# Optimization experiments

Hardware: AMD Instinct MI355X
Metric: run time of the kernel (lower is better)

Reference implementation:

```python
import jax, jax.numpy as jnp
import numpy as np

N = 10000      # atoms
E = 320000     # edges (avg degree 32)
H = 128        # hidden_channels
NH = 8         # num_heads
HD = H // NH   # head_dim
CUTOFF = 5.0


def setup_inputs() -> dict:
    key = jax.random.key(0)
    ks = jax.random.split(key, 32)
    s = 0.05
    x = jax.random.normal(ks[0], (N, H), dtype=jnp.float32)
    vec = jax.random.normal(ks[1], (N, 3, H), dtype=jnp.float32) * 0.1
    edge_index = jax.random.randint(ks[2], (2, E), 0, N, dtype=jnp.int64)
    r_ij = jax.random.uniform(ks[3], (E,), dtype=jnp.float32) * CUTOFF
    f_ij = jax.random.normal(ks[4], (E, H), dtype=jnp.float32)
    d = jax.random.normal(ks[5], (E, 3), dtype=jnp.float32)
    d_ij = d / jnp.linalg.norm(d, axis=-1, keepdims=True)
    def w(k, shape):
        return jax.random.normal(k, shape, dtype=jnp.float32) * s
    params = dict(
        Wq=w(ks[6], (H, H)), bq=jnp.zeros((H,), jnp.float32),
        Wk=w(ks[7], (H, H)), bk=jnp.zeros((H,), jnp.float32),
        Wv=w(ks[8], (H, H)), bv=jnp.zeros((H,), jnp.float32),
        Wdk=w(ks[9], (H, H)), bdk=jnp.zeros((H,), jnp.float32),
        Wdv=w(ks[10], (H, H)), bdv=jnp.zeros((H,), jnp.float32),
        Wvec=w(ks[11], (H, 3 * H)),
        Ws=w(ks[12], (H, 2 * H)), bs=jnp.zeros((2 * H,), jnp.float32),
        Wo=w(ks[13], (H, 3 * H)), bo=jnp.zeros((3 * H,), jnp.float32),
        Wf=w(ks[14], (H, 2 * H)), bf=jnp.zeros((2 * H,), jnp.float32),
        Wwsrc=w(ks[15], (H, H)), Wwtrg=w(ks[16], (H, H)),
        Wtsrc=w(ks[17], (H, H)), Wttrg=w(ks[18], (H, H)),
    )
    return dict(x=x, vec=vec, edge_index=edge_index, r_ij=r_ij,
                f_ij=f_ij, d_ij=d_ij, **params)


def _cosine_cutoff(r):
    return 0.5 * (jnp.cos(r * (jnp.pi / CUTOFF)) + 1.0) * (r < CUTOFF)


def _vector_rejection(v, d):
    # v: [E,3,H], d: [E,3]
    vp = jnp.sum(v * d[:, :, None], axis=1, keepdims=True)  # [E,1,H]
    return v - vp * d[:, :, None]


def reference(x, vec, edge_index, r_ij, f_ij, d_ij,
              Wq, bq, Wk, bk, Wv, bv, Wdk, bdk, Wdv, bdv, Wvec,
              Ws, bs, Wo, bo, Wf, bf, Wwsrc, Wwtrg, Wtsrc, Wttrg):
    silu = jax.nn.silu
    src, dst = edge_index[0], edge_index[1]  # j = source, i = target

    q = (x @ Wq + bq).reshape(-1, NH, HD)
    k = (x @ Wk + bk).reshape(-1, NH, HD)
    v = (x @ Wv + bv).reshape(-1, NH, HD)
    dk = silu(f_ij @ Wdk + bdk).reshape(-1, NH, HD)
    dv = silu(f_ij @ Wdv + bdv).reshape(-1, NH, HD)

    vec1, vec2, vec3 = jnp.split(vec @ Wvec, 3, axis=-1)  # each [N,3,H]
    vec_dot = jnp.sum(vec1 * vec2, axis=1)  # [N,H]

    # message
    attn = jnp.sum(q[dst] * k[src] * dk, axis=-1)          # [E,NH]
    attn = silu(attn) * _cosine_cutoff(r_ij)[:, None]       # [E,NH]
    vj = (v[src] * dv * attn[:, :, None]).reshape(-1, H)    # [E,H]
    s1, s2 = jnp.split(silu(vj @ Ws + bs), 2, axis=-1)
    vec_msg = vec[src] * s1[:, None, :] + s2[:, None, :] * d_ij[:, :, None]  # [E,3,H]

    # aggregate (scatter-add at target node)
    x_agg = jax.ops.segment_sum(vj, dst, num_segments=N)          # [N,H]
    vec_agg = jax.ops.segment_sum(vec_msg, dst, num_segments=N)   # [N,3,H]

    o1, o2, o3 = jnp.split(x_agg @ Wo + bo, 3, axis=-1)
    dx = vec_dot * o2 + o3
    dvec = vec3 * o1[:, None, :] + vec_agg

    # edge update
    vi, vj_full = vec[dst], vec[src]
    w1 = _vector_rejection(vi @ Wwtrg, d_ij)
    w2 = _vector_rejection(vj_full @ Wwsrc, -d_ij)
    w_dot = jnp.sum(w1 * w2, axis=1)  # [E,H]
    t1 = _vector_rejection(vi @ Wttrg, d_ij)
    t2 = _vector_rejection(vi @ Wtsrc, -d_ij)
    t_dot = jnp.sum(t1 * t2, axis=1)  # [E,H]
    f1, f2 = jnp.split(silu(f_ij @ Wf + bf), 2, axis=-1)
    df_ij = f1 * w_dot + f2 * t_dot

    return dx, dvec, df_ij
```

## Files before the change

### kernel.cpp

```cpp
#include <hip/hip_runtime.h>
#include <math.h>

#define NATOM 10000
#define NEDGE 320000
#define HDIM  128
#define NHEAD 8

__device__ __forceinline__ float silu_f(float x) {
    return x / (1.0f + expf(-x));
}

__global__ __launch_bounds__(256) void k_zero4(float4* __restrict__ p, int n4) {
    int i = blockIdx.x * 256 + threadIdx.x;
    if (i < n4) p[i] = float4{0.f, 0.f, 0.f, 0.f};
}

__global__ __launch_bounds__(256) void k_node_qkv(
    const float* __restrict__ x,
    const float* __restrict__ Wq, const float* __restrict__ bq,
    const float* __restrict__ Wk, const float* __restrict__ bk,
    const float* __restrict__ Wv, const float* __restrict__ bv,
    float* __restrict__ q, float* __restrict__ k, float* __restrict__ v)
{
    __shared__ float xs[8 * HDIM];
    int base = blockIdx.x * 8;
    reinterpret_cast<float4*>(xs)[threadIdx.x] =
        reinterpret_cast<const float4*>(x + (size_t)base * HDIM)[threadIdx.x];
    __syncthreads();
    int h = threadIdx.x & 127, half = threadIdx.x >> 7;
    float aq[4], ak[4], av[4];
#pragma unroll
    for (int i = 0; i < 4; ++i) { aq[i] = bq[h]; ak[i] = bk[h]; av[i] = bv[h]; }
    for (int kk = 0; kk < HDIM; ++kk) {
        float wq = Wq[kk * HDIM + h], wk = Wk[kk * HDIM + h], wv = Wv[kk * HDIM + h];
#pragma unroll
        for (int i = 0; i < 4; ++i) {
            float xv = xs[(half + 2 * i) * HDIM + kk];
            aq[i] = fmaf(xv, wq, aq[i]);
            ak[i] = fmaf(xv, wk, ak[i]);
            av[i] = fmaf(xv, wv, av[i]);
        }
    }
#pragma unroll
    for (int i = 0; i < 4; ++i) {
        int node = base + half + 2 * i;
        q[(size_t)node * HDIM + h] = aq[i];
        k[(size_t)node * HDIM + h] = ak[i];
        v[(size_t)node * HDIM + h] = av[i];
    }
}

__global__ __launch_bounds__(256) void k_node_vec(
    const float* __restrict__ vec,
    const float* __restrict__ Wvec,
    const float* __restrict__ Wwtrg, const float* __restrict__ Wwsrc,
    const float* __restrict__ Wttrg, const float* __restrict__ Wtsrc,
    float* __restrict__ vecdot, float* __restrict__ vec3o,
    float* __restrict__ vwt, float* __restrict__ vws,
    float* __restrict__ vtt, float* __restrict__ vts)
{
    __shared__ float vs[8 * 3 * HDIM];
    int base = blockIdx.x * 8;
    {
        const float4* vg = reinterpret_cast<const float4*>(vec + (size_t)base * 3 * HDIM);
        float4* vs4 = reinterpret_cast<float4*>(vs);
        for (int t = threadIdx.x; t < 768; t += 256) vs4[t] = vg[t];
    }
    __syncthreads();
    int h = threadIdx.x & 127, half = threadIdx.x >> 7;
    float vdot[4] = {0.f, 0.f, 0.f, 0.f};
    for (int s = 0; s < 3; ++s) {
        float a1[4] = {0,0,0,0}, a2[4] = {0,0,0,0}, a3[4] = {0,0,0,0};
        float awt[4] = {0,0,0,0}, aws[4] = {0,0,0,0}, att[4] = {0,0,0,0}, ats[4] = {0,0,0,0};
        for (int kk = 0; kk < HDIM; ++kk) {
            float w1 = Wvec[kk * 384 + h];
            float w2 = Wvec[kk * 384 + HDIM + h];
            float w3 = Wvec[kk * 384 + 2 * HDIM + h];
            float wwt = Wwtrg[kk * HDIM + h];
            float wws = Wwsrc[kk * HDIM + h];
            float wtt = Wttrg[kk * HDIM + h];
            float wts = Wtsrc[kk * HDIM + h];
#pragma unroll
            for (int i = 0; i < 4; ++i) {
                float vv = vs[((half + 2 * i) * 3 + s) * HDIM + kk];
                a1[i]  = fmaf(vv, w1, a1[i]);
                a2[i]  = fmaf(vv, w2, a2[i]);
                a3[i]  = fmaf(vv, w3, a3[i]);
                awt[i] = fmaf(vv, wwt, awt[i]);
                aws[i] = fmaf(vv, wws, aws[i]);
                att[i] = fmaf(vv, wtt, att[i]);
                ats[i] = fmaf(vv, wts, ats[i]);
            }
        }
#pragma unroll
        for (int i = 0; i < 4; ++i) {
            int node = base + half + 2 * i;
            size_t ob = ((size_t)node * 3 + s) * HDIM + h;
            vdot[i] += a1[i] * a2[i];
            vec3o[ob] = a3[i];
            vwt[ob] = awt[i];
            vws[ob] = aws[i];
            vtt[ob] = att[i];
            vts[ob] = ats[i];
        }
    }
#pragma unroll
    for (int i = 0; i < 4; ++i)
        vecdot[(size_t)(base + half + 2 * i) * HDIM + h] = vdot[i];
}

__global__ __launch_bounds__(256) void k_edge_fused(
    const float* __restrict__ fij, const int* __restrict__ eidx,
    const float* __restrict__ rij, const float* __restrict__ dij,
    const float* __restrict__ q, const float* __restrict__ k, const float* __restrict__ v,
    const float* __restrict__ vec,
    const float* __restrict__ Wdk, const float* __restrict__ bdk,
    const float* __restrict__ Wdv, const float* __restrict__ bdv,
    const float* __restrict__ Ws, const float* __restrict__ bs,
    float* __restrict__ xagg, float* __restrict__ dvec)
{
    __shared__ float ldsA[16 * 256];
    __shared__ float ldsW[32 * 256];
    __shared__ int   srcS[64], dstS[64];
    __shared__ float rcutS[64];
    __shared__ float dS[64][3];

    int e0 = blockIdx.x * 64;
    if (threadIdx.x < 64) {
        srcS[threadIdx.x] = eidx[e0 + threadIdx.x];
        dstS[threadIdx.x] = eidx[NEDGE + e0 + threadIdx.x];
        float r = rij[e0 + threadIdx.x];
        rcutS[threadIdx.x] = (r < 5.0f) ? 0.5f * (cosf(r * 0.6283185307179586f) + 1.0f) : 0.0f;
    }
    if (threadIdx.x < 192) ((float*)dS)[threadIdx.x] = dij[(size_t)e0 * 3 + threadIdx.x];

    int tx = threadIdx.x & 31, ty = threadIdx.x >> 5;
    float acc[8][8];
#pragma unroll
    for (int i = 0; i < 8; ++i)
#pragma unroll
        for (int j = 0; j < 8; ++j) acc[i][j] = 0.f;

    for (int kc = 0; kc < 4; ++kc) {
#pragma unroll
        for (int it = 0; it < 2; ++it) {
            int f4 = threadIdx.x + it * 256;
            int m = f4 >> 3, c4 = f4 & 7;
            reinterpret_cast<float4*>(ldsA)[f4] =
                *reinterpret_cast<const float4*>(&fij[(size_t)(e0 + m) * HDIM + kc * 32 + c4 * 4]);
        }
#pragma unroll
        for (int it = 0; it < 8; ++it) {
            int f4 = threadIdx.x + it * 256;
            int kk = f4 >> 6, oc4 = f4 & 63;
            int o = oc4 * 4;
            const float* sp = (o < HDIM) ? &Wdk[(size_t)(kc * 32 + kk) * HDIM + o]
                                         : &Wdv[(size_t)(kc * 32 + kk) * HDIM + (o - HDIM)];
            reinterpret_cast<float4*>(ldsW)[f4] = *reinterpret_cast<const float4*>(sp);
        }
        __syncthreads();
#pragma unroll 4
        for (int kk = 0; kk < 32; ++kk) {
            float a[8], b[8];
#pragma unroll
            for (int i = 0; i < 8; ++i) a[i] = ldsA[(ty * 8 + i) * 32 + kk];
#pragma unroll
            for (int j = 0; j < 8; ++j) b[j] = ldsW[kk * 256 + tx + 32 * j];
#pragma unroll
            for (int i = 0; i < 8; ++i)
#pragma unroll
                for (int j = 0; j < 8; ++j) acc[i][j] = fmaf(a[i], b[j], acc[i][j]);
        }
        __syncthreads();
    }

    float bdk_r[4], bdv_r[4];
#pragma unroll
    for (int j = 0; j < 4; ++j) {
        int c = tx + 32 * j;
        bdk_r[j] = bdk[c];
        bdv_r[j] = bdv[c];
    }

    float attn[8][4];
#pragma unroll
    for (int i = 0; i < 8; ++i) {
        int m = ty * 8 + i;
        int sn = srcS[m], dn = dstS[m];
        float rc = rcutS[m];
#pragma unroll
        for (int j = 0; j < 4; ++j) {
            int c = tx + 32 * j;
            float dk = silu_f(acc[i][j] + bdk_r[j]);
            float p = q[(size_t)dn * HDIM + c] * k[(size_t)sn * HDIM + c] * dk;
            p += __shfl_xor(p, 1);
            p += __shfl_xor(p, 2);
            p += __shfl_xor(p, 4);
            p += __shfl_xor(p, 8);
            attn[i][j] = silu_f(p) * rc;
        }
    }

#pragma unroll
    for (int i = 0; i < 8; ++i) {
        int m = ty * 8 + i;
        int sn = srcS[m], dn = dstS[m];
#pragma unroll
        for (int j = 0; j < 4; ++j) {
            int c = tx + 32 * j;
            float dv = silu_f(acc[i][j + 4] + bdv_r[j]);
            float val = v[(size_t)sn * HDIM + c] * dv * attn[i][j];
            ldsW[m * HDIM + c] = val;
            atomicAdd(&xagg[(size_t)dn * HDIM + c], val);
        }
    }
    __syncthreads();

#pragma unroll
    for (int i = 0; i < 8; ++i)
#pragma unroll
        for (int j = 0; j < 8; ++j) acc[i][j] = 0.f;

    for (int kc = 0; kc < 8; ++kc) {
#pragma unroll
        for (int it = 0; it < 4; ++it) {
            int f4 = threadIdx.x + it * 256;
            int kk = f4 >> 6, oc4 = f4 & 63;
            reinterpret_cast<float4*>(ldsA)[f4] =
                reinterpret_cast<const float4*>(Ws)[(size_t)(kc * 16 + kk) * 64 + oc4];
        }
        __syncthreads();
#pragma unroll 4
        for (int kk = 0; kk < 16; ++kk) {
            float a[8], b[8];
#pragma unroll
            for (int i = 0; i < 8; ++i) a[i] = ldsW[(ty * 8 + i) * HDIM + kc * 16 + kk];
#pragma unroll
            for (int j = 0; j < 8; ++j) b[j] = ldsA[kk * 256 + tx + 32 * j];
#pragma unroll
            for (int i = 0; i < 8; ++i)
#pragma unroll
                for (int j = 0; j < 8; ++j) acc[i][j] = fmaf(a[i], b[j], acc[i][j]);
        }
        __syncthreads();
    }

    float bs1[4], bs2[4];
#pragma unroll
    for (int j = 0; j < 4; ++j) {
        int c = tx + 32 * j;
        bs1[j] = bs[c];
        bs2[j] = bs[HDIM + c];
    }
#pragma unroll
    for (int i = 0; i < 8; ++i) {
        int m = ty * 8 + i;
        int dn = dstS[m], sn = srcS[m];
        float d0 = dS[m][0], d1 = dS[m][1], d2 = dS[m][2];
#pragma unroll
        for (int j = 0; j < 4; ++j) {
            int c = tx + 32 * j;
            float s1 = silu_f(acc[i][j] + bs1[j]);
            float s2 = silu_f(acc[i][j + 4] + bs2[j]);
            size_t vb = (size_t)sn * 3 * HDIM + c;
            size_t ab = (size_t)dn * 3 * HDIM + c;
            atomicAdd(&dvec[ab],            fmaf(vec[vb],            s1, s2 * d0));
            atomicAdd(&dvec[ab + HDIM],     fmaf(vec[vb + HDIM],     s1, s2 * d1));
            atomicAdd(&dvec[ab + 2 * HDIM], fmaf(vec[vb + 2 * HDIM], s1, s2 * d2));
        }
    }
}

__global__ __launch_bounds__(256) void k_node_out(
    const float* __restrict__ xagg,
    const float* __restrict__ vecdot, const float* __restrict__ vec3o,
    const float* __restrict__ Wo, const float* __restrict__ bo,
    float* __restrict__ dx, float* __restrict__ dvec)
{
    __shared__ float xs[8 * HDIM];
    int base = blockIdx.x * 8;
    reinterpret_cast<float4*>(xs)[threadIdx.x] =
        reinterpret_cast<const float4*>(xagg + (size_t)base * HDIM)[threadIdx.x];
    __syncthreads();
    int h = threadIdx.x & 127, half = threadIdx.x >> 7;
    float o1[4], o2[4], o3[4];
#pragma unroll
    for (int i = 0; i < 4; ++i) { o1[i] = bo[h]; o2[i] = bo[HDIM + h]; o3[i] = bo[2 * HDIM + h]; }
    for (int kk = 0; kk < HDIM; ++kk) {
        float w1 = Wo[kk * 384 + h], w2 = Wo[kk * 384 + HDIM + h], w3 = Wo[kk * 384 + 2 * HDIM + h];
#pragma unroll
        for (int i = 0; i < 4; ++i) {
            float xv = xs[(half + 2 * i) * HDIM + kk];
            o1[i] = fmaf(xv, w1, o1[i]);
            o2[i] = fmaf(xv, w2, o2[i]);
            o3[i] = fmaf(xv, w3, o3[i]);
        }
    }
#pragma unroll
    for (int i = 0; i < 4; ++i) {
        int node = base + half + 2 * i;
        dx[(size_t)node * HDIM + h] = fmaf(vecdot[(size_t)node * HDIM + h], o2[i], o3[i]);
        size_t vb = (size_t)node * 3 * HDIM + h;
#pragma unroll
        for (int s = 0; s < 3; ++s)
            dvec[vb + s * HDIM] = fmaf(vec3o[vb + s * HDIM], o1[i], dvec[vb + s * HDIM]);
    }
}

__global__ __launch_bounds__(256) void k_edge_df(
    const float* __restrict__ fij, const int* __restrict__ eidx,
    const float* __restrict__ dij,
    const float* __restrict__ Wf, const float* __restrict__ bf,
    const float* __restrict__ vwt, const float* __restrict__ vws,
    const float* __restrict__ vtt, const float* __restrict__ vts,
    float* __restrict__ dfo)
{
    __shared__ float ldsA[64 * HDIM];
    __shared__ float ldsW[16 * 256];
    __shared__ int   srcS[64], dstS[64];
    __shared__ float dS[64][3];

    int e0 = blockIdx.x * 64;
    if (threadIdx.x < 64) {
        srcS[threadIdx.x] = eidx[e0 + threadIdx.x];
        dstS[threadIdx.x] = eidx[NEDGE + e0 + threadIdx.x];
    }
    if (threadIdx.x < 192) ((float*)dS)[threadIdx.x] = dij[(size_t)e0 * 3 + threadIdx.x];
#pragma unroll
    for (int it = 0; it < 8; ++it) {
        int f4 = threadIdx.x + it * 256;
        reinterpret_cast<float4*>(ldsA)[f4] =
            reinterpret_cast<const float4*>(fij + (size_t)e0 * HDIM)[f4];
    }
    __syncthreads();

    int tx = threadIdx.x & 31, ty = threadIdx.x >> 5;
    float acc[8][8];
#pragma unroll
    for (int i = 0; i < 8; ++i)
#pragma unroll
        for (int j = 0; j < 8; ++j) acc[i][j] = 0.f;

    for (int kc = 0; kc < 8; ++kc) {
#pragma unroll
        for (int it = 0; it < 4; ++it) {
            int f4 = threadIdx.x + it * 256;
            int kk = f4 >> 6, oc4 = f4 & 63;
            reinterpret_cast<float4*>(ldsW)[f4] =
                reinterpret_cast<const float4*>(Wf)[(size_t)(kc * 16 + kk) * 64 + oc4];
        }
        __syncthreads();
#pragma unroll 4
        for (int kk = 0; kk < 16; ++kk) {
            float a[8], b[8];
#pragma unroll
            for (int i = 0; i < 8; ++i) a[i] = ldsA[(ty * 8 + i) * HDIM + kc * 16 + kk];
#pragma unroll
            for (int j = 0; j < 8; ++j) b[j] = ldsW[kk * 256 + tx + 32 * j];
#pragma unroll
            for (int i = 0; i < 8; ++i)
#pragma unroll
                for (int j = 0; j < 8; ++j) acc[i][j] = fmaf(a[i], b[j], acc[i][j]);
        }
        __syncthreads();
    }
    float bf1[4], bf2[4];
#pragma unroll
    for (int j = 0; j < 4; ++j) {
        int c = tx + 32 * j;
        bf1[j] = bf[c];
        bf2[j] = bf[HDIM + c];
    }
#pragma unroll
    for (int i = 0; i < 8; ++i) {
        int m = ty * 8 + i;
        int dn = dstS[m], sn = srcS[m];
        float d0 = dS[m][0], d1 = dS[m][1], d2 = dS[m][2];
#pragma unroll
        for (int j = 0; j < 4; ++j) {
            int c = tx + 32 * j;
            float f1 = silu_f(acc[i][j] + bf1[j]);
            float f2 = silu_f(acc[i][j + 4] + bf2[j]);
            size_t db = (size_t)dn * 3 * HDIM + c;
            size_t sb = (size_t)sn * 3 * HDIM + c;
            float a0 = vwt[db], a1 = vwt[db + HDIM], a2 = vwt[db + 2 * HDIM];
            float b0 = vws[sb], b1 = vws[sb + HDIM], b2 = vws[sb + 2 * HDIM];
            float t10 = vtt[db], t11 = vtt[db + HDIM], t12 = vtt[db + 2 * HDIM];
            float t20 = vts[db], t21 = vts[db + HDIM], t22 = vts[db + 2 * HDIM];
            float A  = a0 * d0 + a1 * d1 + a2 * d2;
            float B  = b0 * d0 + b1 * d1 + b2 * d2;
            float P1 = t10 * d0 + t11 * d1 + t12 * d2;
            float P2 = t20 * d0 + t21 * d1 + t22 * d2;
            float wdot = a0 * b0 + a1 * b1 + a2 * b2 - A * B;
            float tdot = t10 * t20 + t11 * t21 + t12 * t22 - P1 * P2;
            dfo[(size_t)(e0 + m) * HDIM + c] = f1 * wdot + f2 * tdot;
        }
    }
}

extern "C" void kernel_launch(void* const* d_in, const int* in_sizes, int n_in,
                              void* d_out, int out_size, void* d_ws, size_t ws_size,
                              hipStream_t stream)
{
    const float* x     = (const float*)d_in[0];
    const float* vec   = (const float*)d_in[1];
    const int*   eidx  = (const int*)d_in[2];
    const float* rij   = (const float*)d_in[3];
    const float* fij   = (const float*)d_in[4];
    const float* dij   = (const float*)d_in[5];
    const float* Wq    = (const float*)d_in[6];
    const float* bq    = (const float*)d_in[7];
    const float* Wk    = (const float*)d_in[8];
    const float* bk    = (const float*)d_in[9];
    const float* Wv    = (const float*)d_in[10];
    const float* bv    = (const float*)d_in[11];
    const float* Wdk   = (const float*)d_in[12];
    const float* bdk   = (const float*)d_in[13];
    const float* Wdv   = (const float*)d_in[14];
    const float* bdv   = (const float*)d_in[15];
    const float* Wvec  = (const float*)d_in[16];
    const float* Ws    = (const float*)d_in[17];
    const float* bs    = (const float*)d_in[18];
    const float* Wo    = (const float*)d_in[19];
    const float* bo    = (const float*)d_in[20];
    const float* Wf    = (const float*)d_in[21];
    const float* bf    = (const float*)d_in[22];
    const float* Wwsrc = (const float*)d_in[23];
    const float* Wwtrg = (const float*)d_in[24];
    const float* Wtsrc = (const float*)d_in[25];
    const float* Wttrg = (const float*)d_in[26];

    float* ws = (float*)d_ws;
    size_t o = 0;
    float* q      = ws + o; o += (size_t)NATOM * HDIM;
    float* kf     = ws + o; o += (size_t)NATOM * HDIM;
    float* vf     = ws + o; o += (size_t)NATOM * HDIM;
    float* vecdot = ws + o; o += (size_t)NATOM * HDIM;
    float* vec3o  = ws + o; o += (size_t)NATOM * 3 * HDIM;
    float* vwt    = ws + o; o += (size_t)NATOM * 3 * HDIM;
    float* vws_   = ws + o; o += (size_t)NATOM * 3 * HDIM;
    float* vtt    = ws + o; o += (size_t)NATOM * 3 * HDIM;
    float* vts    = ws + o; o += (size_t)NATOM * 3 * HDIM;
    float* xagg   = ws + o; o += (size_t)NATOM * HDIM;

    float* dx   = (float*)d_out;
    float* dvec = dx + (size_t)NATOM * HDIM;
    float* dfo  = dvec + (size_t)NATOM * 3 * HDIM;

    hipLaunchKernelGGL(k_zero4, dim3((NATOM * HDIM / 4 + 255) / 256), dim3(256), 0, stream,
                       (float4*)xagg, NATOM * HDIM / 4);
    hipLaunchKernelGGL(k_zero4, dim3((NATOM * 3 * HDIM / 4 + 255) / 256), dim3(256), 0, stream,
                       (float4*)dvec, NATOM * 3 * HDIM / 4);
    hipLaunchKernelGGL(k_node_qkv, dim3(NATOM / 8), dim3(256), 0, stream,
                       x, Wq, bq, Wk, bk, Wv, bv, q, kf, vf);
    hipLaunchKernelGGL(k_node_vec, dim3(NATOM / 8), dim3(256), 0, stream,
                       vec, Wvec, Wwtrg, Wwsrc, Wttrg, Wtsrc,
                       vecdot, vec3o, vwt, vws_, vtt, vts);
    hipLaunchKernelGGL(k_edge_fused, dim3(NEDGE / 64), dim3(256), 0, stream,
                       fij, eidx, rij, dij, q, kf, vf, vec,
                       Wdk, bdk, Wdv, bdv, Ws, bs, xagg, dvec);
    hipLaunchKernelGGL(k_node_out, dim3(NATOM / 8), dim3(256), 0, stream,
                       xagg, vecdot, vec3o, Wo, bo, dx, dvec);
    hipLaunchKernelGGL(k_edge_df, dim3(NEDGE / 64), dim3(256), 0, stream,
                       fij, eidx, dij, Wf, bf, vwt, vws_, vtt, vts, dfo);
}
```

Before: 1.689 ms.

## Fuse edge kernels and run edge GEMMs on bf16x3 split MFMA

Merges the two edge kernels into one, so f_ij is read and converted only once per edge tile. The three per-edge GEMMs (Wf, Wdk/Wdv and Ws) move from scalar FP32 FMA loops to MFMA 16x16x32 bf16 instructions. Inputs and weights are split into high and low bf16 parts, and three products are summed to keep near-FP32 accuracy. A prep kernel converts and transposes the weights each call. This trades more MFMA work and LDS conversion for far cheaper matrix math and one fewer kernel launch.

```diff
diff --git a/kernel.cpp b/kernel.cpp
--- a/kernel.cpp
+++ b/kernel.cpp
@@ -6,13 +6,47 @@
 #define HDIM  128
 #define NHEAD 8
 
+typedef short  v8s  __attribute__((ext_vector_type(8)));
+typedef float  v4f  __attribute__((ext_vector_type(4)));
+
 __device__ __forceinline__ float silu_f(float x) {
     return x / (1.0f + expf(-x));
+}
+
+__device__ __forceinline__ short f2bf(float x) {
+    union { float f; unsigned u; } c; c.f = x;
+    unsigned r = (c.u + 0x7FFF + ((c.u >> 16) & 1)) >> 16;
+    return (short)r;
+}
+__device__ __forceinline__ float bf2f(short h) {
+    union { unsigned u; float f; } c; c.u = ((unsigned)(unsigned short)h) << 16;
+    return c.f;
 }
 
 __global__ __launch_bounds__(256) void k_zero4(float4* __restrict__ p, int n4) {
     int i = blockIdx.x * 256 + threadIdx.x;
     if (i < n4) p[i] = float4{0.f, 0.f, 0.f, 0.f};
+}
+
+__global__ __launch_bounds__(128) void k_prep(
+    const float* __restrict__ Wdk, const float* __restrict__ Wdv,
+    const float* __restrict__ Ws,  const float* __restrict__ Wf,
+    short* __restrict__ WmsgH, short* __restrict__ WmsgL,
+    short* __restrict__ WstH,  short* __restrict__ WstL,
+    short* __restrict__ WftH,  short* __restrict__ WftL)
+{
+    int b = blockIdx.x;
+    int mat = b >> 8, n = b & 255, k = threadIdx.x;
+    float x;
+    if (mat == 0) x = (n < HDIM) ? Wdk[k * HDIM + n] : Wdv[k * HDIM + (n - HDIM)];
+    else if (mat == 1) x = Ws[k * 256 + n];
+    else x = Wf[k * 256 + n];
+    short h = f2bf(x);
+    short l = f2bf(x - bf2f(h));
+    short* H = (mat == 0) ? WmsgH : (mat == 1) ? WstH : WftH;
+    short* L = (mat == 0) ? WmsgL : (mat == 1) ? WstL : WftL;
+    H[n * HDIM + k] = h;
+    L[n * HDIM + k] = l;
 }
 
 __global__ __launch_bounds__(256) void k_node_qkv(
@@ -109,164 +143,194 @@
         vecdot[(size_t)(base + half + 2 * i) * HDIM + h] = vdot[i];
 }
 
-__global__ __launch_bounds__(256) void k_edge_fused(
+__device__ __forceinline__ void gemm_split(
+    const short* asHp, const short* asLp,
+    const short* __restrict__ WH, const short* __restrict__ WL,
+    const int* colbase, int n16, int q8, v4f acc[4][4])
+{
+#pragma unroll
+    for (int kc = 0; kc < 4; ++kc) {
+        v8s aH[4], aL[4];
+#pragma unroll
+        for (int mt = 0; mt < 4; ++mt) {
+            int off = (mt * 16 + n16) * 136 + kc * 32 + q8 * 8;
+            aH[mt] = *reinterpret_cast<const v8s*>(asHp + off);
+            aL[mt] = *reinterpret_cast<const v8s*>(asLp + off);
+        }
+#pragma unroll
+        for (int nt = 0; nt < 4; ++nt) {
+            size_t woff = (size_t)(colbase[nt] + n16) * HDIM + kc * 32 + q8 * 8;
+            v8s bH = *reinterpret_cast<const v8s*>(WH + woff);
+            v8s bL = *reinterpret_cast<const v8s*>(WL + woff);
+#pragma unroll
+            for (int mt = 0; mt < 4; ++mt) {
+                acc[mt][nt] = __builtin_amdgcn_mfma_f32_16x16x32_bf16(aH[mt], bL, acc[mt][nt], 0, 0, 0);
+                acc[mt][nt] = __builtin_amdgcn_mfma_f32_16x16x32_bf16(aL[mt], bH, acc[mt][nt], 0, 0, 0);
+                acc[mt][nt] = __builtin_amdgcn_mfma_f32_16x16x32_bf16(aH[mt], bH, acc[mt][nt], 0, 0, 0);
+            }
+        }
+    }
+}
+
+__global__ __launch_bounds__(256) void k_edge_mega(
     const float* __restrict__ fij, const int* __restrict__ eidx,
     const float* __restrict__ rij, const float* __restrict__ dij,
     const float* __restrict__ q, const float* __restrict__ k, const float* __restrict__ v,
     const float* __restrict__ vec,
-    const float* __restrict__ Wdk, const float* __restrict__ bdk,
-    const float* __restrict__ Wdv, const float* __restrict__ bdv,
-    const float* __restrict__ Ws, const float* __restrict__ bs,
-    float* __restrict__ xagg, float* __restrict__ dvec)
-{
-    __shared__ float ldsA[16 * 256];
-    __shared__ float ldsW[32 * 256];
+    const short* __restrict__ WmsgH, const short* __restrict__ WmsgL,
+    const short* __restrict__ WstH,  const short* __restrict__ WstL,
+    const short* __restrict__ WftH,  const short* __restrict__ WftL,
+    const float* __restrict__ bdk, const float* __restrict__ bdv,
+    const float* __restrict__ bs,  const float* __restrict__ bfb,
+    const float* __restrict__ vwt, const float* __restrict__ vws,
+    const float* __restrict__ vtt, const float* __restrict__ vts,
+    float* __restrict__ xagg, float* __restrict__ dvec, float* __restrict__ dfo)
+{
+    __shared__ short asH[64 * 136];
+    __shared__ short asL[64 * 136];
     __shared__ int   srcS[64], dstS[64];
-    __shared__ float rcutS[64];
-    __shared__ float dS[64][3];
+    __shared__ float rcutS[64], d0S[64], d1S[64], d2S[64];
 
     int e0 = blockIdx.x * 64;
     if (threadIdx.x < 64) {
-        srcS[threadIdx.x] = eidx[e0 + threadIdx.x];
-        dstS[threadIdx.x] = eidx[NEDGE + e0 + threadIdx.x];
-        float r = rij[e0 + threadIdx.x];
-        rcutS[threadIdx.x] = (r < 5.0f) ? 0.5f * (cosf(r * 0.6283185307179586f) + 1.0f) : 0.0f;
-    }
-    if (threadIdx.x < 192) ((float*)dS)[threadIdx.x] = dij[(size_t)e0 * 3 + threadIdx.x];
-
-    int tx = threadIdx.x & 31, ty = threadIdx.x >> 5;
-    float acc[8][8];
-#pragma unroll
-    for (int i = 0; i < 8; ++i)
-#pragma unroll
-        for (int j = 0; j < 8; ++j) acc[i][j] = 0.f;
-
-    for (int kc = 0; kc < 4; ++kc) {
-#pragma unroll
-        for (int it = 0; it < 2; ++it) {
-            int f4 = threadIdx.x + it * 256;
-            int m = f4 >> 3, c4 = f4 & 7;
-            reinterpret_cast<float4*>(ldsA)[f4] =
-                *reinterpret_cast<const float4*>(&fij[(size_t)(e0 + m) * HDIM + kc * 32 + c4 * 4]);
-        }
-#pragma unroll
-        for (int it = 0; it < 8; ++it) {
-            int f4 = threadIdx.x + it * 256;
-            int kk = f4 >> 6, oc4 = f4 & 63;
-            int o = oc4 * 4;
-            const float* sp = (o < HDIM) ? &Wdk[(size_t)(kc * 32 + kk) * HDIM + o]
-                                         : &Wdv[(size_t)(kc * 32 + kk) * HDIM + (o - HDIM)];
-            reinterpret_cast<float4*>(ldsW)[f4] = *reinterpret_cast<const float4*>(sp);
-        }
-        __syncthreads();
-#pragma unroll 4
-        for (int kk = 0; kk < 32; ++kk) {
-            float a[8], b[8];
-#pragma unroll
-            for (int i = 0; i < 8; ++i) a[i] = ldsA[(ty * 8 + i) * 32 + kk];
-#pragma unroll
-            for (int j = 0; j < 8; ++j) b[j] = ldsW[kk * 256 + tx + 32 * j];
-#pragma unroll
-            for (int i = 0; i < 8; ++i)
-#pragma unroll
-                for (int j = 0; j < 8; ++j) acc[i][j] = fmaf(a[i], b[j], acc[i][j]);
-        }
-        __syncthreads();
-    }
-
-    float bdk_r[4], bdv_r[4];
-#pragma unroll
-    for (int j = 0; j < 4; ++j) {
-        int c = tx + 32 * j;
-        bdk_r[j] = bdk[c];
-        bdv_r[j] = bdv[c];
-    }
-
-    float attn[8][4];
-#pragma unroll
-    for (int i = 0; i < 8; ++i) {
-        int m = ty * 8 + i;
-        int sn = srcS[m], dn = dstS[m];
-        float rc = rcutS[m];
-#pragma unroll
-        for (int j = 0; j < 4; ++j) {
-            int c = tx + 32 * j;
-            float dk = silu_f(acc[i][j] + bdk_r[j]);
-            float p = q[(size_t)dn * HDIM + c] * k[(size_t)sn * HDIM + c] * dk;
-            p += __shfl_xor(p, 1);
-            p += __shfl_xor(p, 2);
-            p += __shfl_xor(p, 4);
-            p += __shfl_xor(p, 8);
-            attn[i][j] = silu_f(p) * rc;
-        }
-    }
-
-#pragma unroll
-    for (int i = 0; i < 8; ++i) {
-        int m = ty * 8 + i;
-        int sn = srcS[m], dn = dstS[m];
-#pragma unroll
-        for (int j = 0; j < 4; ++j) {
-            int c = tx + 32 * j;
-            float dv = silu_f(acc[i][j + 4] + bdv_r[j]);
-            float val = v[(size_t)sn * HDIM + c] * dv * attn[i][j];
-            ldsW[m * HDIM + c] = val;
-            atomicAdd(&xagg[(size_t)dn * HDIM + c], val);
-        }
-    }
-    __syncthreads();
-
-#pragma unroll
-    for (int i = 0; i < 8; ++i)
-#pragma unroll
-        for (int j = 0; j < 8; ++j) acc[i][j] = 0.f;
-
-    for (int kc = 0; kc < 8; ++kc) {
-#pragma unroll
-        for (int it = 0; it < 4; ++it) {
-            int f4 = threadIdx.x + it * 256;
-            int kk = f4 >> 6, oc4 = f4 & 63;
-            reinterpret_cast<float4*>(ldsA)[f4] =
-                reinterpret_cast<const float4*>(Ws)[(size_t)(kc * 16 + kk) * 64 + oc4];
-        }
-        __syncthreads();
-#pragma unroll 4
-        for (int kk = 0; kk < 16; ++kk) {
-            float a[8], b[8];
-#pragma unroll
-            for (int i = 0; i < 8; ++i) a[i] = ldsW[(ty * 8 + i) * HDIM + kc * 16 + kk];
-#pragma unroll
-            for (int j = 0; j < 8; ++j) b[j] = ldsA[kk * 256 + tx + 32 * j];
-#pragma unroll
-            for (int i = 0; i < 8; ++i)
-#pragma unroll
-                for (int j = 0; j < 8; ++j) acc[i][j] = fmaf(a[i], b[j], acc[i][j]);
-        }
-        __syncthreads();
-    }
-
-    float bs1[4], bs2[4];
-#pragma unroll
-    for (int j = 0; j < 4; ++j) {
-        int c = tx + 32 * j;
-        bs1[j] = bs[c];
-        bs2[j] = bs[HDIM + c];
-    }
-#pragma unroll
-    for (int i = 0; i < 8; ++i) {
-        int m = ty * 8 + i;
-        int dn = dstS[m], sn = srcS[m];
-        float d0 = dS[m][0], d1 = dS[m][1], d2 = dS[m][2];
-#pragma unroll
-        for (int j = 0; j < 4; ++j) {
-            int c = tx + 32 * j;
-            float s1 = silu_f(acc[i][j] + bs1[j]);
-            float s2 = silu_f(acc[i][j + 4] + bs2[j]);
-            size_t vb = (size_t)sn * 3 * HDIM + c;
-            size_t ab = (size_t)dn * 3 * HDIM + c;
-            atomicAdd(&dvec[ab],            fmaf(vec[vb],            s1, s2 * d0));
-            atomicAdd(&dvec[ab + HDIM],     fmaf(vec[vb + HDIM],     s1, s2 * d1));
-            atomicAdd(&dvec[ab + 2 * HDIM], fmaf(vec[vb + 2 * HDIM], s1, s2 * d2));
+        int t = threadIdx.x;
+        srcS[t] = eidx[e0 + t];
+        dstS[t] = eidx[NEDGE + e0 + t];
+        float r = rij[e0 + t];
+        rcutS[t] = (r < 5.0f) ? 0.5f * (cosf(r * 0.6283185307179586f) + 1.0f) : 0.0f;
+        d0S[t] = dij[(size_t)(e0 + t) * 3 + 0];
+        d1S[t] = dij[(size_t)(e0 + t) * 3 + 1];
+        d2S[t] = dij[(size_t)(e0 + t) * 3 + 2];
+    }
+
+    {
+        int m  = threadIdx.x >> 2;
+        int q4 = threadIdx.x & 3;
+        const float4* src = reinterpret_cast<const float4*>(fij + (size_t)(e0 + m) * HDIM + q4 * 32);
+        short* hp = &asH[m * 136 + q4 * 32];
+        short* lp = &asL[m * 136 + q4 * 32];
+#pragma unroll
+        for (int c8 = 0; c8 < 4; ++c8) {
+            float4 x0 = src[c8 * 2], x1 = src[c8 * 2 + 1];
+            float xs[8] = {x0.x, x0.y, x0.z, x0.w, x1.x, x1.y, x1.z, x1.w};
+            v8s hv, lv;
+#pragma unroll
+            for (int j = 0; j < 8; ++j) {
+                short h = f2bf(xs[j]);
+                hv[j] = h;
+                lv[j] = f2bf(xs[j] - bf2f(h));
+            }
+            *reinterpret_cast<v8s*>(hp + c8 * 8) = hv;
+            *reinterpret_cast<v8s*>(lp + c8 * 8) = lv;
+        }
+    }
+    __syncthreads();
+
+    int lane = threadIdx.x & 63;
+    int wv   = threadIdx.x >> 6;
+    int n16  = lane & 15;
+    int q8   = lane >> 4;
+    int colbase[4] = {wv * 32, wv * 32 + 16, 128 + wv * 32, 128 + wv * 32 + 16};
+
+    v4f acc[4][4];
+
+#pragma unroll
+    for (int mt = 0; mt < 4; ++mt)
+#pragma unroll
+        for (int nt = 0; nt < 4; ++nt) acc[mt][nt] = v4f{0.f, 0.f, 0.f, 0.f};
+    gemm_split(asH, asL, WftH, WftL, colbase, n16, q8, acc);
+
+#pragma unroll
+    for (int nt2 = 0; nt2 < 2; ++nt2) {
+        int c1 = colbase[nt2] + n16;
+        float bf1 = bfb[c1], bf2 = bfb[HDIM + c1];
+#pragma unroll
+        for (int mt = 0; mt < 4; ++mt) {
+#pragma unroll
+            for (int r = 0; r < 4; ++r) {
+                int m  = mt * 16 + q8 * 4 + r;
+                int dn = dstS[m], sn = srcS[m];
+                float d0 = d0S[m], d1 = d1S[m], d2 = d2S[m];
+                float f1 = silu_f(acc[mt][nt2][r] + bf1);
+                float f2 = silu_f(acc[mt][nt2 + 2][r] + bf2);
+                size_t db = (size_t)dn * 384 + c1;
+                size_t sb = (size_t)sn * 384 + c1;
+                float a0 = vwt[db], a1 = vwt[db + HDIM], a2 = vwt[db + 2 * HDIM];
+                float b0 = vws[sb], b1 = vws[sb + HDIM], b2 = vws[sb + 2 * HDIM];
+                float t10 = vtt[db], t11 = vtt[db + HDIM], t12 = vtt[db + 2 * HDIM];
+                float t20 = vts[db], t21 = vts[db + HDIM], t22 = vts[db + 2 * HDIM];
+                float A  = a0 * d0 + a1 * d1 + a2 * d2;
+                float B  = b0 * d0 + b1 * d1 + b2 * d2;
+                float P1 = t10 * d0 + t11 * d1 + t12 * d2;
+                float P2 = t20 * d0 + t21 * d1 + t22 * d2;
+                float wdot = a0 * b0 + a1 * b1 + a2 * b2 - A * B;
+                float tdot = t10 * t20 + t11 * t21 + t12 * t22 - P1 * P2;
+                dfo[(size_t)(e0 + m) * HDIM + c1] = f1 * wdot + f2 * tdot;
+            }
+        }
+    }
+
+#pragma unroll
+    for (int mt = 0; mt < 4; ++mt)
+#pragma unroll
+        for (int nt = 0; nt < 4; ++nt) acc[mt][nt] = v4f{0.f, 0.f, 0.f, 0.f};
+    gemm_split(asH, asL, WmsgH, WmsgL, colbase, n16, q8, acc);
+
+    __syncthreads();
+
+#pragma unroll
+    for (int nt2 = 0; nt2 < 2; ++nt2) {
+        int c1 = colbase[nt2] + n16;
+        float bdk1 = bdk[c1], bdv1 = bdv[c1];
+#pragma unroll
+        for (int mt = 0; mt < 4; ++mt) {
+#pragma unroll
+            for (int r = 0; r < 4; ++r) {
+                int m  = mt * 16 + q8 * 4 + r;
+                int dn = dstS[m], sn = srcS[m];
+                float dk = silu_f(acc[mt][nt2][r] + bdk1);
+                float p = q[(size_t)dn * HDIM + c1] * k[(size_t)sn * HDIM + c1] * dk;
+                p += __shfl_xor(p, 1);
+                p += __shfl_xor(p, 2);
+                p += __shfl_xor(p, 4);
+                p += __shfl_xor(p, 8);
+                float at = silu_f(p) * rcutS[m];
+                float dv = silu_f(acc[mt][nt2 + 2][r] + bdv1);
+                float vjv = v[(size_t)sn * HDIM + c1] * dv * at;
+                atomicAdd(&xagg[(size_t)dn * HDIM + c1], vjv);
+                short h = f2bf(vjv);
+                asH[m * 136 + c1] = h;
+                asL[m * 136 + c1] = f2bf(vjv - bf2f(h));
+            }
+        }
+    }
+    __syncthreads();
+
+#pragma unroll
+    for (int mt = 0; mt < 4; ++mt)
+#pragma unroll
+        for (int nt = 0; nt < 4; ++nt) acc[mt][nt] = v4f{0.f, 0.f, 0.f, 0.f};
+    gemm_split(asH, asL, WstH, WstL, colbase, n16, q8, acc);
+
+#pragma unroll
+    for (int nt2 = 0; nt2 < 2; ++nt2) {
+        int c1 = colbase[nt2] + n16;
+        float bs1 = bs[c1], bs2 = bs[HDIM + c1];
+#pragma unroll
+        for (int mt = 0; mt < 4; ++mt) {
+#pragma unroll
+            for (int r = 0; r < 4; ++r) {
+                int m  = mt * 16 + q8 * 4 + r;
+                int dn = dstS[m], sn = srcS[m];
+                float d0 = d0S[m], d1 = d1S[m], d2 = d2S[m];
+                float s1 = silu_f(acc[mt][nt2][r] + bs1);
+                float s2 = silu_f(acc[mt][nt2 + 2][r] + bs2);
+                size_t vb = (size_t)sn * 384 + c1;
+                size_t ab = (size_t)dn * 384 + c1;
+                atomicAdd(&dvec[ab],            fmaf(vec[vb],            s1, s2 * d0));
+                atomicAdd(&dvec[ab + HDIM],     fmaf(vec[vb + HDIM],     s1, s2 * d1));
+                atomicAdd(&dvec[ab + 2 * HDIM], fmaf(vec[vb + 2 * HDIM], s1, s2 * d2));
+            }
         }
     }
 }
@@ -304,97 +368,6 @@
 #pragma unroll
         for (int s = 0; s < 3; ++s)
             dvec[vb + s * HDIM] = fmaf(vec3o[vb + s * HDIM], o1[i], dvec[vb + s * HDIM]);
-    }
-}
-
-__global__ __launch_bounds__(256) void k_edge_df(
-    const float* __restrict__ fij, const int* __restrict__ eidx,
-    const float* __restrict__ dij,
-    const float* __restrict__ Wf, const float* __restrict__ bf,
-    const float* __restrict__ vwt, const float* __restrict__ vws,
-    const float* __restrict__ vtt, const float* __restrict__ vts,
-    float* __restrict__ dfo)
-{
-    __shared__ float ldsA[64 * HDIM];
-    __shared__ float ldsW[16 * 256];
-    __shared__ int   srcS[64], dstS[64];
-    __shared__ float dS[64][3];
-
-    int e0 = blockIdx.x * 64;
-    if (threadIdx.x < 64) {
-        srcS[threadIdx.x] = eidx[e0 + threadIdx.x];
-        dstS[threadIdx.x] = eidx[NEDGE + e0 + threadIdx.x];
-    }
-    if (threadIdx.x < 192) ((float*)dS)[threadIdx.x] = dij[(size_t)e0 * 3 + threadIdx.x];
-#pragma unroll
-    for (int it = 0; it < 8; ++it) {
-        int f4 = threadIdx.x + it * 256;
-        reinterpret_cast<float4*>(ldsA)[f4] =
-            reinterpret_cast<const float4*>(fij + (size_t)e0 * HDIM)[f4];
-    }
-    __syncthreads();
-
-    int tx = threadIdx.x & 31, ty = threadIdx.x >> 5;
-    float acc[8][8];
-#pragma unroll
-    for (int i = 0; i < 8; ++i)
-#pragma unroll
-        for (int j = 0; j < 8; ++j) acc[i][j] = 0.f;
-
-    for (int kc = 0; kc < 8; ++kc) {
-#pragma unroll
-        for (int it = 0; it < 4; ++it) {
-            int f4 = threadIdx.x + it * 256;
-            int kk = f4 >> 6, oc4 = f4 & 63;
-            reinterpret_cast<float4*>(ldsW)[f4] =
-                reinterpret_cast<const float4*>(Wf)[(size_t)(kc * 16 + kk) * 64 + oc4];
-        }
-        __syncthreads();
-#pragma unroll 4
-        for (int kk = 0; kk < 16; ++kk) {
-            float a[8], b[8];
-#pragma unroll
-            for (int i = 0; i < 8; ++i) a[i] = ldsA[(ty * 8 + i) * HDIM + kc * 16 + kk];
-#pragma unroll
-            for (int j = 0; j < 8; ++j) b[j] = ldsW[kk * 256 + tx + 32 * j];
-#pragma unroll
-            for (int i = 0; i < 8; ++i)
-#pragma unroll
-                for (int j = 0; j < 8; ++j) acc[i][j] = fmaf(a[i], b[j], acc[i][j]);
-        }
-        __syncthreads();
-    }
-    float bf1[4], bf2[4];
-#pragma unroll
-    for (int j = 0; j < 4; ++j) {
-        int c = tx + 32 * j;
-        bf1[j] = bf[c];
-        bf2[j] = bf[HDIM + c];
-    }
-#pragma unroll
-    for (int i = 0; i < 8; ++i) {
-        int m = ty * 8 + i;
-        int dn = dstS[m], sn = srcS[m];
-        float d0 = dS[m][0], d1 = dS[m][1], d2 = dS[m][2];
-#pragma unroll
-        for (int j = 0; j < 4; ++j) {
-            int c = tx + 32 * j;
-            float f1 = silu_f(acc[i][j] + bf1[j]);
-            float f2 = silu_f(acc[i][j + 4] + bf2[j]);
-            size_t db = (size_t)dn * 3 * HDIM + c;
-            size_t sb = (size_t)sn * 3 * HDIM + c;
-            float a0 = vwt[db], a1 = vwt[db + HDIM], a2 = vwt[db + 2 * HDIM];
-            float b0 = vws[sb], b1 = vws[sb + HDIM], b2 = vws[sb + 2 * HDIM];
-            float t10 = vtt[db], t11 = vtt[db + HDIM], t12 = vtt[db + 2 * HDIM];
-            float t20 = vts[db], t21 = vts[db + HDIM], t22 = vts[db + 2 * HDIM];
-            float A  = a0 * d0 + a1 * d1 + a2 * d2;
-            float B  = b0 * d0 + b1 * d1 + b2 * d2;
-            float P1 = t10 * d0 + t11 * d1 + t12 * d2;
-            float P2 = t20 * d0 + t21 * d1 + t22 * d2;
-            float wdot = a0 * b0 + a1 * b1 + a2 * b2 - A * B;
-            float tdot = t10 * t20 + t11 * t21 + t12 * t22 - P1 * P2;
-            dfo[(size_t)(e0 + m) * HDIM + c] = f1 * wdot + f2 * tdot;
-        }
     }
 }
 
@@ -442,11 +415,22 @@
     float* vtt    = ws + o; o += (size_t)NATOM * 3 * HDIM;
     float* vts    = ws + o; o += (size_t)NATOM * 3 * HDIM;
     float* xagg   = ws + o; o += (size_t)NATOM * HDIM;
+    short* WmsgH = (short*)(ws + o); o += 16384 / 2 * 1;
+    o -= 16384 / 2;
+    short* wbase = (short*)(ws + o);
+    WmsgH = wbase + 0 * 32768;
+    short* WmsgL = wbase + 1 * 32768;
+    short* WstH  = wbase + 2 * 32768;
+    short* WstL  = wbase + 3 * 32768;
+    short* WftH  = wbase + 4 * 32768;
+    short* WftL  = wbase + 5 * 32768;
 
     float* dx   = (float*)d_out;
     float* dvec = dx + (size_t)NATOM * HDIM;
     float* dfo  = dvec + (size_t)NATOM * 3 * HDIM;
 
+    hipLaunchKernelGGL(k_prep, dim3(768), dim3(128), 0, stream,
+                       Wdk, Wdv, Ws, Wf, WmsgH, WmsgL, WstH, WstL, WftH, WftL);
     hipLaunchKernelGGL(k_zero4, dim3((NATOM * HDIM / 4 + 255) / 256), dim3(256), 0, stream,
                        (float4*)xagg, NATOM * HDIM / 4);
     hipLaunchKernelGGL(k_zero4, dim3((NATOM * 3 * HDIM / 4 + 255) / 256), dim3(256), 0, stream,
@@ -456,11 +440,12 @@
     hipLaunchKernelGGL(k_node_vec, dim3(NATOM / 8), dim3(256), 0, stream,
                        vec, Wvec, Wwtrg, Wwsrc, Wttrg, Wtsrc,
                        vecdot, vec3o, vwt, vws_, vtt, vts);
-    hipLaunchKernelGGL(k_edge_fused, dim3(NEDGE / 64), dim3(256), 0, stream,
+    hipLaunchKernelGGL(k_edge_mega, dim3(NEDGE / 64), dim3(256), 0, stream,
                        fij, eidx, rij, dij, q, kf, vf, vec,
-                       Wdk, bdk, Wdv, bdv, Ws, bs, xagg, dvec);
+                       WmsgH, WmsgL, WstH, WstL, WftH, WftL,
+                       bdk, bdv, bs, bf,
+                       vwt, vws_, vtt, vts,
+                       xagg, dvec, dfo);
     hipLaunchKernelGGL(k_node_out, dim3(NATOM / 8), dim3(256), 0, stream,
                        xagg, vecdot, vec3o, Wo, bo, dx, dvec);
-    hipLaunchKernelGGL(k_edge_df, dim3(NEDGE / 64), dim3(256), 0, stream,
-                       fij, eidx, dij, Wf, bf, vwt, vws_, vtt, vts, dfo);
-}
+}
```

Measured after the change: 2.414 ms. 1.43x slower.
